# Performance work log

Measured on AMD Instinct MI355X. Metric: run time of the kernel, lower is better.

## Reference

```python
import jax, jax.numpy as jnp
import numpy as np
from jax import lax

VOCAB = 28996  # bert-base-cased vocab size (static for segment_sum)
B, S, D = 32, 512, 768
NUM_CLASSES = 9


def _lstm_dir(x, w_ih, w_hh, b_ih, b_hh):
    # x: [T, N, In]; torch gate order i, f, g, o packed along dim 0 of weights
    T, N, _ = x.shape
    H = w_hh.shape[1]
    xg = jnp.einsum('tni,gi->tng', x, w_ih) + b_ih  # precompute input projections [T,N,4H]

    def step(carry, xg_t):
        h, c = carry
        g = xg_t + h @ w_hh.T + b_hh
        i, f, gg, o = jnp.split(g, 4, axis=-1)
        c = jax.nn.sigmoid(f) * c + jax.nn.sigmoid(i) * jnp.tanh(gg)
        h = jax.nn.sigmoid(o) * jnp.tanh(c)
        return (h, c), h

    h0 = jnp.zeros((N, H), x.dtype)
    _, ys = lax.scan(step, (h0, h0), xg)
    return ys  # [T, N, H]


def setup_inputs() -> dict:
    key = jax.random.key(0)
    ks = jax.random.split(key, 8)
    H, In = D, 2 * D
    w = 0.02
    return {
        'batch': jax.random.randint(ks[0], (B, S), 0, VOCAB),
        'hidden': jax.random.normal(ks[1], (B, S, D), jnp.float32),
        'w_ih_f': jax.random.normal(ks[2], (4 * H, In), jnp.float32) * w,
        'w_hh_f': jax.random.normal(ks[3], (4 * H, H), jnp.float32) * w,
        'b_ih_f': jnp.zeros((4 * H,), jnp.float32),
        'b_hh_f': jnp.zeros((4 * H,), jnp.float32),
        'w_ih_b': jax.random.normal(ks[4], (4 * H, In), jnp.float32) * w,
        'w_hh_b': jax.random.normal(ks[5], (4 * H, H), jnp.float32) * w,
        'b_ih_b': jnp.zeros((4 * H,), jnp.float32),
        'b_hh_b': jnp.zeros((4 * H,), jnp.float32),
        'lin_w': jax.random.normal(ks[6], (NUM_CLASSES, 2 * H), jnp.float32) * w,
        'lin_b': jnp.zeros((NUM_CLASSES,), jnp.float32),
    }


def reference(batch, hidden, w_ih_f, w_hh_f, b_ih_f, b_hh_f,
              w_ih_b, w_hh_b, b_ih_b, b_hh_b, lin_w, lin_b):
    b, s, d = hidden.shape
    flat_ids = batch.reshape(-1)            # [B*S]
    flat_h = hidden.reshape(-1, d)          # [B*S, D]
    # segment mean of embeddings grouped by raw token id (the dict loop in torch)
    sums = jax.ops.segment_sum(flat_h, flat_ids, num_segments=VOCAB)
    counts = jax.ops.segment_sum(jnp.ones((flat_ids.shape[0], 1), hidden.dtype),
                                 flat_ids, num_segments=VOCAB)
    means = sums / jnp.maximum(counts, 1.0)
    ctx = means[flat_ids].reshape(b, s, d)  # gather-broadcast back per position
    x = jnp.concatenate([hidden, ctx], axis=2)  # [B, S, 2D]
    # nn.LSTM is not batch_first: scans over dim0 (B acts as time, S as batch)
    out_f = _lstm_dir(x, w_ih_f, w_hh_f, b_ih_f, b_hh_f)
    out_b = _lstm_dir(x[::-1], w_ih_b, w_hh_b, b_ih_b, b_hh_b)[::-1]
    out = jnp.concatenate([out_f, out_b], axis=-1)  # [B, S, 2D]
    # dropout is identity in eval mode
    return out @ lin_w.T + lin_b  # [B, S, num_classes]
```

## Files before the change

kernel.cpp:

```cpp
#include <hip/hip_runtime.h>

#define VOCAB 28996
#define BB 32
#define SS 512
#define DD 768
#define NCLS 9
#define ROWS (BB*SS)
#define IN2 (2*DD)
#define G4 (4*DD)
#define NB2 (2*G4)

typedef __attribute__((ext_vector_type(8))) short short8;
typedef __attribute__((ext_vector_type(4))) short shortx4;
typedef __attribute__((ext_vector_type(4))) float floatx4;
typedef unsigned long long ull;

__device__ __forceinline__ float bf2f(unsigned short u){
  union { unsigned int i; float f; } v; v.i = ((unsigned int)u) << 16; return v.f;
}
__device__ __forceinline__ unsigned short f2bf(float f){
  union { float f; unsigned int i; } v; v.f = f;
  unsigned int r = v.i + 0x7FFFu + ((v.i >> 16) & 1u);
  return (unsigned short)(r >> 16);
}
__device__ __forceinline__ float sigf(float x){ return 1.0f / (1.0f + __expf(-x)); }
__device__ __forceinline__ float tanhfast(float x){
  float y = fminf(fmaxf(x, -15.f), 15.f);
  float e = __expf(2.f * y);
  return 1.f - 2.f / (e + 1.f);
}

__device__ __forceinline__ void gl_lds16(const unsigned short* g, unsigned short* l){
  __builtin_amdgcn_global_load_lds((__attribute__((address_space(1))) void*)(g),
                                   (__attribute__((address_space(3))) void*)(l), 16, 0, 0);
}
__device__ __forceinline__ void gl_lds16_c(const unsigned short* g, unsigned short* l){
  __builtin_amdgcn_global_load_lds((__attribute__((address_space(1))) void*)(g),
                                   (__attribute__((address_space(3))) void*)(l), 16, 0, 17);
}
__device__ __forceinline__ void store16_sc1(unsigned short* p, short8 v){
  asm volatile("global_store_dwordx4 %0, %1, off sc0 sc1" :: "v"(p), "v"(v) : "memory");
}

#define VMCNT(n) do { asm volatile("s_waitcnt vmcnt(" #n ")" ::: "memory"); \
                      __builtin_amdgcn_sched_barrier(0); } while (0)

__global__ void seg_scatter(const int* __restrict__ ids, const float* __restrict__ hidden,
                            float* __restrict__ sums, float* __restrict__ counts)
{
  int r = blockIdx.x;
  int id = ids[r];
  const float* h = hidden + (long)r * DD;
  float* s = sums + (long)id * DD;
  for (int d = threadIdx.x; d < DD; d += 256)
    atomicAdd(&s[d], h[d]);
  if (threadIdx.x == 0) atomicAdd(&counts[id], 1.0f);
}

__global__ void build_x(const int* __restrict__ ids, const float* __restrict__ hidden,
                        const float* __restrict__ sums, const float* __restrict__ counts,
                        unsigned short* __restrict__ x)
{
  int r = blockIdx.x;
  int id = ids[r];
  float inv = 1.0f / fmaxf(counts[id], 1.0f);
  const float* h = hidden + (long)r * DD;
  const float* s = sums + (long)id * DD;
  unsigned short* xr = x + (long)r * IN2;
  for (int d = threadIdx.x; d < DD; d += 256) {
    xr[d]      = f2bf(h[d]);
    xr[DD + d] = f2bf(s[d] * inv);
  }
}

__global__ void conv_w_perm(const float* __restrict__ w, unsigned short* __restrict__ o, int K)
{
  long i = (long)blockIdx.x * 256 + threadIdx.x;
  if (i >= (long)G4 * K) return;
  int row = (int)(i / K); int k = (int)(i - (long)row * K);
  int u = row >> 2, g = row & 3;
  o[i] = f2bf(w[((long)(g * DD + u)) * K + k]);
}

__global__ void conv_bias_perm(const float* __restrict__ bif, const float* __restrict__ bhf,
                               const float* __restrict__ bib, const float* __restrict__ bhb,
                               float* __restrict__ o)
{
  int n = blockIdx.x * 256 + threadIdx.x;
  if (n >= NB2) return;
  int d = n / G4, rr = n - d * G4, u = rr >> 2, g = rr & 3;
  int s = g * DD + u;
  o[n] = d ? (bib[s] + bhb[s]) : (bif[s] + bhf[s]);
}

__global__ __launch_bounds__(256, 2)
void gemm_bt(const unsigned short* __restrict__ A, int lda,
             const unsigned short* __restrict__ B, int ldb,
             unsigned short* __restrict__ C, int ldc,
             const float* __restrict__ bias, int K)
{
  __shared__ unsigned short lA[128 * 32];
  __shared__ unsigned short lB[128 * 32];
  const int t = threadIdx.x;
  const int lane = t & 63;
  const int wv = t >> 6;
  const int wm = wv >> 1, wn = wv & 1;
  const int l15 = lane & 15, q = lane >> 4;
  const long m0 = (long)blockIdx.y * 128;
  const long n0 = (long)blockIdx.x * 128;
  const int rowS = t >> 2;
  const int kc = (((t & 3) ^ ((t >> 3) & 3))) * 8;
  const int qsw = (q ^ ((l15 >> 1) & 3)) * 8;
  const unsigned short* gA = A + (m0 + rowS) * lda + kc;
  const unsigned short* gB = B + (n0 + rowS) * ldb + kc;
  unsigned short* dA0 = lA + (wv << 9);
  unsigned short* dA1 = lA + 2048 + (wv << 9);
  unsigned short* dB0 = lB + (wv << 9);
  unsigned short* dB1 = lB + 2048 + (wv << 9);

  floatx4 acc[4][4];
  #pragma unroll
  for (int i = 0; i < 4; i++)
    #pragma unroll
    for (int j = 0; j < 4; j++)
      acc[i][j] = (floatx4){0.f, 0.f, 0.f, 0.f};

  const long a64 = (long)64 * lda;
  const long b64 = (long)64 * ldb;
  for (int kt = 0; kt < K; kt += 32) {
    gl_lds16(gA + kt,       dA0);
    gl_lds16(gA + a64 + kt, dA1);
    gl_lds16(gB + kt,       dB0);
    gl_lds16(gB + b64 + kt, dB1);
    __syncthreads();
    short8 af[4], bfr[4];
    #pragma unroll
    for (int i = 0; i < 4; i++)
      af[i] = *(const short8*)(lA + (wm * 64 + i * 16 + l15) * 32 + qsw);
    #pragma unroll
    for (int j = 0; j < 4; j++)
      bfr[j] = *(const short8*)(lB + (wn * 64 + j * 16 + l15) * 32 + qsw);
    #pragma unroll
    for (int i = 0; i < 4; i++)
      #pragma unroll
      for (int j = 0; j < 4; j++)
        acc[i][j] = __builtin_amdgcn_mfma_f32_16x16x32_bf16(af[i], bfr[j], acc[i][j], 0, 0, 0);
    __syncthreads();
  }

  #pragma unroll
  for (int i = 0; i < 4; i++) {
    #pragma unroll
    for (int j = 0; j < 4; j++) {
      const long mg = m0 + wm * 64 + i * 16 + q * 4;
      const long ng = n0 + wn * 64 + j * 16 + l15;
      const float bb = bias[ng];
      #pragma unroll
      for (int r = 0; r < 4; r++)
        C[(mg + r) * ldc + ng] = f2bf(acc[i][j][r] + bb);
    }
  }
}

__global__ __launch_bounds__(512, 1)
void lstm_persist(const unsigned short* __restrict__ xg, int ldxg,
                  const unsigned short* __restrict__ whh,
                  unsigned short* __restrict__ hbuf,
                  unsigned short* __restrict__ outc,
                  unsigned* bar,
                  int dir0, int ndir)
{
  __shared__ unsigned short bufA[16384];
  __shared__ unsigned short bufB[16384];
  __shared__ unsigned short xgs[2][16384];
  __shared__ unsigned short hout[128 * 40];

  const int bid = blockIdx.x;
  const int xcd = bid & 7;
  const int idx = bid >> 3;
  int dm, k3;
  if (ndir == 2) { dm = idx & 7; k3 = idx >> 3; }
  else           { dm = idx & 3; k3 = idx >> 2; }
  const int ld  = (ndir == 2) ? (dm & 1) : 0;
  const int dir = dir0 + ld;
  const int mt  = (ndir == 2) ? (dm >> 1) : dm;
  const int nt  = k3 * 8 + xcd;
  const int m0 = mt * 128, n0 = nt * 128;
  const int u0 = n0 >> 2;
  unsigned* gbar = bar + dm * 16;
  const int nb24 = 24;

  const int t0 = threadIdx.x;
  const int lane = t0 & 63;
  const int wv = t0 >> 6;
  const int wm = wv >> 1;
  const int wn = wv & 1;
  const int l15 = lane & 15, q = lane >> 4;
  const long ldoff = (ndir == 2 && ld == 1) ? (long)G4 : 0;

  const unsigned short* Bdir = whh + (long)dir * G4 * DD;
  const int srow  = lane >> 2;
  const int scolA = (((lane & 3) ^ ((lane >> 3) & 3))) * 8;
  const int qsw   = (q ^ ((l15 >> 1) & 3)) * 8;
  const int xsw   = l15 << 3;
  const int xsrc  = (((t0 & 15) ^ ((t0 >> 4) & 15))) * 8;

  const int rb = wv * 16 + srow;
  const unsigned short* wB  = Bdir + (long)(n0 + rb) * DD + scolA;
  const unsigned short* hA0 = hbuf + ((long)0 * ndir + ld) * ((long)SS * DD) + (long)(m0 + rb) * DD + scolA;
  const unsigned short* hA1 = hbuf + ((long)1 * ndir + ld) * ((long)SS * DD) + (long)(m0 + rb) * DD + scolA;
  unsigned short* dstA = bufA + wv * 512 + lane * 8;
  unsigned short* dstB = bufB + wv * 512 + lane * 8;

  float c_reg[2][4];
  #pragma unroll
  for (int i = 0; i < 2; i++)
    #pragma unroll
    for (int j = 0; j < 4; j++)
      c_reg[i][j] = 0.f;

  {
    const int tt0 = dir ? (BB - 1) : 0;
    const unsigned short* xrow = xg + ((long)tt0 * SS + m0) * ldxg + ldoff + n0;
    #pragma unroll
    for (int c = 0; c < 4; c++) {
      int row = c * 32 + (t0 >> 4);
      gl_lds16(xrow + (long)row * ldxg + xsrc,
               xgs[0] + c * 4096 + (t0 >> 4) * 128 + (t0 & 15) * 8);
    }
  }

  for (int s = 0; s < BB; s++) {
    const int tt = dir ? (BB - 1 - s) : s;
    const unsigned short* hA = (s & 1) ? hA1 : hA0;
    unsigned short* hw = hbuf + (((long)((s + 1) & 1)) * ndir + ld) * ((long)SS * DD);
    const unsigned short* xcur = xgs[s & 1];

    {
      gl_lds16_c(hA,        dstA);
      gl_lds16_c(hA + 32,   dstA + 4096);
      gl_lds16 (wB,         dstB);
      gl_lds16 (wB + 32,    dstB + 4096);
      gl_lds16_c(hA + 64,   dstA + 8192);
      gl_lds16_c(hA + 96,   dstA + 12288);
      gl_lds16 (wB + 64,    dstB + 8192);
      gl_lds16 (wB + 96,    dstB + 12288);
      if (s < BB - 1) {
        const int tn = dir ? (BB - 2 - s) : (s + 1);
        const unsigned short* xrow = xg + ((long)tn * SS + m0) * ldxg + ldoff + n0;
        unsigned short* xnxt = xgs[(s + 1) & 1];
        #pragma unroll
        for (int c = 0; c < 4; c++) {
          int row = c * 32 + (t0 >> 4);
          gl_lds16(xrow + (long)row * ldxg + xsrc,
                   xnxt + c * 4096 + (t0 >> 4) * 128 + (t0 & 15) * 8);
        }
      }
    }
    VMCNT(8);
    __builtin_amdgcn_s_barrier();

    floatx4 acc[2][4];
    #pragma unroll
    for (int i = 0; i < 2; i++)
      #pragma unroll
      for (int j = 0; j < 4; j++)
        acc[i][j] = (floatx4){0.f, 0.f, 0.f, 0.f};

    #pragma unroll
    for (int kt = 0; kt < 12; kt++) {
      const int cur = kt & 1;
      const unsigned short* pA = bufA + cur * 8192;
      const unsigned short* pB = bufB + cur * 8192;
      #pragma unroll
      for (int ks = 0; ks < 2; ks++) {
        short8 af[2], bfr[4];
        #pragma unroll
        for (int i = 0; i < 2; i++)
          af[i] = *(const short8*)(pA + ks * 4096 + (wm * 32 + i * 16 + l15) * 32 + qsw);
        #pragma unroll
        for (int j = 0; j < 4; j++)
          bfr[j] = *(const short8*)(pB + ks * 4096 + (wn * 64 + j * 16 + l15) * 32 + qsw);
        #pragma unroll
        for (int i = 0; i < 2; i++)
          #pragma unroll
          for (int j = 0; j < 4; j++)
            acc[i][j] = __builtin_amdgcn_mfma_f32_16x16x32_bf16(bfr[j], af[i], acc[i][j], 0, 0, 0);
      }
      __builtin_amdgcn_s_barrier();
      if (kt < 10) {
        const long kb = (long)(kt + 2) * 64;
        unsigned short* dA = bufA + cur * 8192 + wv * 512 + lane * 8;
        unsigned short* dB = bufB + cur * 8192 + wv * 512 + lane * 8;
        gl_lds16_c(hA + kb,      dA);
        gl_lds16_c(hA + kb + 32, dA + 4096);
        gl_lds16 (wB + kb,      dB);
        gl_lds16 (wB + kb + 32, dB + 4096);
        VMCNT(4);
        __builtin_amdgcn_s_barrier();
      } else if (kt == 10) {
        VMCNT(0);
        __builtin_amdgcn_s_barrier();
      }
    }

    #pragma unroll
    for (int i = 0; i < 2; i++) {
      const int mrow = wm * 32 + i * 16 + l15;
      const int xbase = mrow * 128;
      #pragma unroll
      for (int j = 0; j < 4; j++) {
        const int nb = wn * 64 + j * 16 + q * 4;
        shortx4 xv = *(const shortx4*)(xcur + xbase + (nb ^ xsw));
        float gi = acc[i][j][0] + bf2f((unsigned short)xv[0]);
        float gf = acc[i][j][1] + bf2f((unsigned short)xv[1]);
        float gg = acc[i][j][2] + bf2f((unsigned short)xv[2]);
        float go = acc[i][j][3] + bf2f((unsigned short)xv[3]);
        float c = sigf(gf) * c_reg[i][j] + sigf(gi) * tanhfast(gg);
        float h = sigf(go) * tanhfast(c);
        c_reg[i][j] = c;
        hout[mrow * 40 + (nb >> 2)] = f2bf(h);
      }
    }
    __syncthreads();
    {
      const int row = t0 >> 2;
      const int qq = t0 & 3;
      short8 v0 = *(const short8*)(hout + row * 40 + qq * 8);
      unsigned short* hwp = hw + (long)(m0 + row) * DD + u0 + qq * 8;
      unsigned short* op  = outc + ((long)tt * SS + m0 + row) * IN2 + dir * DD + u0 + qq * 8;
      store16_sc1(hwp, v0);
      *(short8*)op = v0;
    }
    if (s < BB - 1) {
      VMCNT(0);
      __builtin_amdgcn_s_barrier();
      if (threadIdx.x == 0) {
        unsigned g = __hip_atomic_load(gbar + 1, __ATOMIC_RELAXED, __HIP_MEMORY_SCOPE_AGENT);
        unsigned a = __hip_atomic_fetch_add(gbar, 1u, __ATOMIC_RELAXED, __HIP_MEMORY_SCOPE_AGENT);
        if (a == (unsigned)(nb24 - 1)) {
          __hip_atomic_store(gbar, 0u, __ATOMIC_RELAXED, __HIP_MEMORY_SCOPE_AGENT);
          __hip_atomic_store(gbar + 1, g + 1u, __ATOMIC_RELEASE, __HIP_MEMORY_SCOPE_AGENT);
        } else {
          unsigned curv;
          do {
            __builtin_amdgcn_s_sleep(2);
            curv = __hip_atomic_load(gbar + 1, __ATOMIC_RELAXED, __HIP_MEMORY_SCOPE_AGENT);
          } while (curv == g);
        }
      }
      __builtin_amdgcn_s_barrier();
    }
  }
}

__global__ void final_linear(const unsigned short* __restrict__ xin, const float* __restrict__ w,
                             const float* __restrict__ b, float* __restrict__ out)
{
  __shared__ float red[NCLS * 256];
  int row = blockIdx.x;
  const unsigned short* x = xin + (long)row * IN2;
  float p[NCLS];
  #pragma unroll
  for (int c = 0; c < NCLS; c++) p[c] = 0.f;
  for (int k = threadIdx.x; k < IN2; k += 256) {
    float xv = bf2f(x[k]);
    #pragma unroll
    for (int c = 0; c < NCLS; c++) p[c] += xv * w[c * IN2 + k];
  }
  #pragma unroll
  for (int c = 0; c < NCLS; c++) red[c * 256 + threadIdx.x] = p[c];
  __syncthreads();
  for (int s = 128; s > 0; s >>= 1) {
    if (threadIdx.x < s) {
      #pragma unroll
      for (int c = 0; c < NCLS; c++)
        red[c * 256 + threadIdx.x] += red[c * 256 + threadIdx.x + s];
    }
    __syncthreads();
  }
  if (threadIdx.x < NCLS)
    out[(long)row * NCLS + threadIdx.x] = red[threadIdx.x * 256] + b[threadIdx.x];
}

extern "C" void kernel_launch(void* const* d_in, const int* in_sizes, int n_in,
                              void* d_out, int out_size, void* d_ws, size_t ws_size,
                              hipStream_t stream)
{
  const int*   batch  = (const int*)d_in[0];
  const float* hidden = (const float*)d_in[1];
  const float* w_ih_f = (const float*)d_in[2];
  const float* w_hh_f = (const float*)d_in[3];
  const float* b_ih_f = (const float*)d_in[4];
  const float* b_hh_f = (const float*)d_in[5];
  const float* w_ih_b = (const float*)d_in[6];
  const float* w_hh_b = (const float*)d_in[7];
  const float* b_ih_b = (const float*)d_in[8];
  const float* b_hh_b = (const float*)d_in[9];
  const float* lin_w  = (const float*)d_in[10];
  const float* lin_b  = (const float*)d_in[11];
  float* out = (float*)d_out;

  char* ws = (char*)d_ws;
  size_t off = 0;
  auto alloc = [&](size_t bytes) -> char* {
    char* p = ws + off;
    off += (bytes + 255) & ~(size_t)255;
    return p;
  };

  const size_t SZ_XG_A = (size_t)ROWS * NB2 * 2;
  const size_t SZ_XG_B = (size_t)ROWS * G4  * 2;
  const size_t SZ_XBF  = (size_t)ROWS * IN2 * 2;
  const size_t SZ_W    = (size_t)G4 * IN2 * 2;
  const size_t SZ_BIAS = (size_t)NB2 * 4;
  const size_t SZ_HBUF = (size_t)2 * 2 * SS * DD * 2;
  const size_t SZ_BAR  = 512;
  const size_t SZ_SUMS = (size_t)VOCAB * DD * 4 + (size_t)VOCAB * 4;

  const size_t NEED_C = SZ_XG_A + SZ_XBF + SZ_W + SZ_BIAS + SZ_HBUF + SZ_BAR + 8 * 256;
  const bool combined = ws_size >= NEED_C;

  const long nWIH = (long)G4 * IN2;
  const long nWHH = (long)G4 * DD;

  if (combined) {
    unsigned short* xg   = (unsigned short*)alloc(SZ_XG_A);
    unsigned short* xbf  = (unsigned short*)alloc(SZ_XBF);
    unsigned short* wbuf = (unsigned short*)alloc(SZ_W);
    float*          bias = (float*)alloc(SZ_BIAS);
    unsigned short* hbuf = (unsigned short*)alloc(SZ_HBUF);
    unsigned*       bar  = (unsigned*)alloc(SZ_BAR);
    float* sums   = (float*)xg;
    float* counts = sums + (size_t)VOCAB * DD;

    hipMemsetAsync(sums, 0, SZ_SUMS, stream);
    hipMemsetAsync(bar, 0, SZ_BAR, stream);
    seg_scatter<<<ROWS, 256, 0, stream>>>(batch, hidden, sums, counts);
    build_x<<<ROWS, 256, 0, stream>>>(batch, hidden, sums, counts, xbf);
    conv_bias_perm<<<(NB2 + 255) / 256, 256, 0, stream>>>(b_ih_f, b_hh_f, b_ih_b, b_hh_b, bias);

    for (int dir = 0; dir < 2; dir++) {
      conv_w_perm<<<(unsigned)((nWIH + 255) / 256), 256, 0, stream>>>(dir ? w_ih_b : w_ih_f, wbuf, IN2);
      dim3 grid(G4 / 128, ROWS / 128, 1);
      gemm_bt<<<grid, 256, 0, stream>>>(xbf, IN2, wbuf, IN2,
                                        xg + (size_t)dir * G4, NB2,
                                        bias + (size_t)dir * G4, IN2);
    }
    conv_w_perm<<<(unsigned)((nWHH + 255) / 256), 256, 0, stream>>>(w_hh_f, wbuf, DD);
    conv_w_perm<<<(unsigned)((nWHH + 255) / 256), 256, 0, stream>>>(w_hh_b, wbuf + (size_t)G4 * DD, DD);

    hipMemsetAsync(hbuf, 0, SZ_HBUF, stream);
    lstm_persist<<<192, 512, 0, stream>>>(xg, NB2, wbuf, hbuf, xbf, bar, 0, 2);
    final_linear<<<ROWS, 256, 0, stream>>>(xbf, lin_w, lin_b, out);
  } else {
    unsigned short* xg   = (unsigned short*)alloc(SZ_XG_B);
    unsigned short* xbf  = (unsigned short*)alloc(SZ_XBF);
    unsigned short* outc = (unsigned short*)alloc(SZ_XBF);
    unsigned short* wih  = (unsigned short*)alloc(SZ_W);
    unsigned short* whh  = (unsigned short*)alloc(SZ_W);
    float*          bias = (float*)alloc(SZ_BIAS);
    unsigned short* hbuf = (unsigned short*)alloc(SZ_HBUF);
    unsigned*       bar  = (unsigned*)alloc(SZ_BAR);
    float* sums   = (float*)xg;
    float* counts = sums + (size_t)VOCAB * DD;

    hipMemsetAsync(sums, 0, SZ_SUMS, stream);
    hipMemsetAsync(bar, 0, SZ_BAR, stream);
    seg_scatter<<<ROWS, 256, 0, stream>>>(batch, hidden, sums, counts);
    build_x<<<ROWS, 256, 0, stream>>>(batch, hidden, sums, counts, xbf);
    conv_bias_perm<<<(NB2 + 255) / 256, 256, 0, stream>>>(b_ih_f, b_hh_f, b_ih_b, b_hh_b, bias);
    conv_w_perm<<<(unsigned)((nWHH + 255) / 256), 256, 0, stream>>>(w_hh_f, whh, DD);
    conv_w_perm<<<(unsigned)((nWHH + 255) / 256), 256, 0, stream>>>(w_hh_b, whh + (size_t)G4 * DD, DD);

    for (int dir = 0; dir < 2; dir++) {
      conv_w_perm<<<(unsigned)((nWIH + 255) / 256), 256, 0, stream>>>(dir ? w_ih_b : w_ih_f, wih, IN2);
      {
        dim3 grid(G4 / 128, ROWS / 128, 1);
        gemm_bt<<<grid, 256, 0, stream>>>(xbf, IN2, wih, IN2, xg, G4,
                                          bias + (size_t)dir * G4, IN2);
      }
      hipMemsetAsync(hbuf, 0, SZ_HBUF, stream);
      lstm_persist<<<96, 512, 0, stream>>>(xg, G4, whh, hbuf, outc, bar, dir, 1);
    }
    final_linear<<<ROWS, 256, 0, stream>>>(outc, lin_w, lin_b, out);
  }
}
```

Measured before the change: 1.225 ms.

## Restructure LSTM recurrent K-loop into 6 double-buffered chunks with register xg loads

The persistent LSTM kernel's per-step recurrent GEMM now uses two full K=128 LDS buffers for h and W_hh instead of split 64-wide halves, giving 6 outer iterations with one prefetch and fewer barriers per iteration. The precomputed input-gate values are loaded straight into registers from global memory rather than staged through a double-buffered LDS array, which frees LDS for the larger h/W buffers. It also raises wave priority around the MFMA section. The direct global loads of xg may be less coalesced and add register pressure, and their latency now sits in the step's critical path instead of being prefetched a step ahead.

```diff
diff --git a/kernel.cpp b/kernel.cpp
--- a/kernel.cpp
+++ b/kernel.cpp
@@ -170,9 +170,8 @@
                   unsigned* bar,
                   int dir0, int ndir)
 {
-  __shared__ unsigned short bufA[16384];
-  __shared__ unsigned short bufB[16384];
-  __shared__ unsigned short xgs[2][16384];
+  __shared__ unsigned short bufA[2][16384];
+  __shared__ unsigned short bufB[2][16384];
   __shared__ unsigned short hout[128 * 40];
 
   const int bid = blockIdx.x;
@@ -202,15 +201,11 @@
   const int srow  = lane >> 2;
   const int scolA = (((lane & 3) ^ ((lane >> 3) & 3))) * 8;
   const int qsw   = (q ^ ((l15 >> 1) & 3)) * 8;
-  const int xsw   = l15 << 3;
-  const int xsrc  = (((t0 & 15) ^ ((t0 >> 4) & 15))) * 8;
 
   const int rb = wv * 16 + srow;
   const unsigned short* wB  = Bdir + (long)(n0 + rb) * DD + scolA;
   const unsigned short* hA0 = hbuf + ((long)0 * ndir + ld) * ((long)SS * DD) + (long)(m0 + rb) * DD + scolA;
   const unsigned short* hA1 = hbuf + ((long)1 * ndir + ld) * ((long)SS * DD) + (long)(m0 + rb) * DD + scolA;
-  unsigned short* dstA = bufA + wv * 512 + lane * 8;
-  unsigned short* dstB = bufB + wv * 512 + lane * 8;
 
   float c_reg[2][4];
   #pragma unroll
@@ -218,47 +213,28 @@
     #pragma unroll
     for (int j = 0; j < 4; j++)
       c_reg[i][j] = 0.f;
-
-  {
-    const int tt0 = dir ? (BB - 1) : 0;
-    const unsigned short* xrow = xg + ((long)tt0 * SS + m0) * ldxg + ldoff + n0;
-    #pragma unroll
-    for (int c = 0; c < 4; c++) {
-      int row = c * 32 + (t0 >> 4);
-      gl_lds16(xrow + (long)row * ldxg + xsrc,
-               xgs[0] + c * 4096 + (t0 >> 4) * 128 + (t0 & 15) * 8);
-    }
-  }
 
   for (int s = 0; s < BB; s++) {
     const int tt = dir ? (BB - 1 - s) : s;
     const unsigned short* hA = (s & 1) ? hA1 : hA0;
     unsigned short* hw = hbuf + (((long)((s + 1) & 1)) * ndir + ld) * ((long)SS * DD);
-    const unsigned short* xcur = xgs[s & 1];
-
+
+    #pragma unroll
+    for (int p = 0; p < 4; p++) {
+      gl_lds16_c(hA + p * 32, &bufA[0][p * 4096 + wv * 512 + lane * 8]);
+      gl_lds16 (wB + p * 32, &bufB[0][p * 4096 + wv * 512 + lane * 8]);
+    }
+    shortx4 xr0[4], xr1[4];
     {
-      gl_lds16_c(hA,        dstA);
-      gl_lds16_c(hA + 32,   dstA + 4096);
-      gl_lds16 (wB,         dstB);
-      gl_lds16 (wB + 32,    dstB + 4096);
-      gl_lds16_c(hA + 64,   dstA + 8192);
-      gl_lds16_c(hA + 96,   dstA + 12288);
-      gl_lds16 (wB + 64,    dstB + 8192);
-      gl_lds16 (wB + 96,    dstB + 12288);
-      if (s < BB - 1) {
-        const int tn = dir ? (BB - 2 - s) : (s + 1);
-        const unsigned short* xrow = xg + ((long)tn * SS + m0) * ldxg + ldoff + n0;
-        unsigned short* xnxt = xgs[(s + 1) & 1];
-        #pragma unroll
-        for (int c = 0; c < 4; c++) {
-          int row = c * 32 + (t0 >> 4);
-          gl_lds16(xrow + (long)row * ldxg + xsrc,
-                   xnxt + c * 4096 + (t0 >> 4) * 128 + (t0 & 15) * 8);
-        }
-      }
-    }
-    VMCNT(8);
-    __builtin_amdgcn_s_barrier();
+      const unsigned short* xb = xg + ((long)tt * SS + m0) * ldxg + ldoff + n0;
+      const unsigned short* xb0 = xb + (long)(wm * 32 + l15) * ldxg + wn * 64 + q * 4;
+      const unsigned short* xb1 = xb0 + (long)16 * ldxg;
+      #pragma unroll
+      for (int j = 0; j < 4; j++) {
+        xr0[j] = *(const shortx4*)(xb0 + j * 16);
+        xr1[j] = *(const shortx4*)(xb1 + j * 16);
+      }
+    }
 
     floatx4 acc[2][4];
     #pragma unroll
@@ -268,50 +244,50 @@
         acc[i][j] = (floatx4){0.f, 0.f, 0.f, 0.f};
 
     #pragma unroll
-    for (int kt = 0; kt < 12; kt++) {
-      const int cur = kt & 1;
-      const unsigned short* pA = bufA + cur * 8192;
-      const unsigned short* pB = bufB + cur * 8192;
-      #pragma unroll
-      for (int ks = 0; ks < 2; ks++) {
+    for (int j6 = 0; j6 < 6; j6++) {
+      if (j6 < 5) {
+        const int b = (j6 + 1) & 1;
+        const long kb = (long)(j6 + 1) * 128;
+        #pragma unroll
+        for (int p = 0; p < 4; p++) {
+          gl_lds16_c(hA + kb + p * 32, &bufA[b][p * 4096 + wv * 512 + lane * 8]);
+          gl_lds16 (wB + kb + p * 32, &bufB[b][p * 4096 + wv * 512 + lane * 8]);
+        }
+      }
+      if (j6 == 0)      VMCNT(16);
+      else if (j6 < 5)  VMCNT(8);
+      else              VMCNT(0);
+      __builtin_amdgcn_s_barrier();
+      const int b = j6 & 1;
+      __builtin_amdgcn_s_setprio(1);
+      #pragma unroll
+      for (int ks = 0; ks < 4; ks++) {
+        const unsigned short* pA = &bufA[b][ks * 4096];
+        const unsigned short* pB = &bufB[b][ks * 4096];
         short8 af[2], bfr[4];
         #pragma unroll
         for (int i = 0; i < 2; i++)
-          af[i] = *(const short8*)(pA + ks * 4096 + (wm * 32 + i * 16 + l15) * 32 + qsw);
+          af[i] = *(const short8*)(pA + (wm * 32 + i * 16 + l15) * 32 + qsw);
         #pragma unroll
         for (int j = 0; j < 4; j++)
-          bfr[j] = *(const short8*)(pB + ks * 4096 + (wn * 64 + j * 16 + l15) * 32 + qsw);
+          bfr[j] = *(const short8*)(pB + (wn * 64 + j * 16 + l15) * 32 + qsw);
         #pragma unroll
         for (int i = 0; i < 2; i++)
           #pragma unroll
           for (int j = 0; j < 4; j++)
             acc[i][j] = __builtin_amdgcn_mfma_f32_16x16x32_bf16(bfr[j], af[i], acc[i][j], 0, 0, 0);
       }
-      __builtin_amdgcn_s_barrier();
-      if (kt < 10) {
-        const long kb = (long)(kt + 2) * 64;
-        unsigned short* dA = bufA + cur * 8192 + wv * 512 + lane * 8;
-        unsigned short* dB = bufB + cur * 8192 + wv * 512 + lane * 8;
-        gl_lds16_c(hA + kb,      dA);
-        gl_lds16_c(hA + kb + 32, dA + 4096);
-        gl_lds16 (wB + kb,      dB);
-        gl_lds16 (wB + kb + 32, dB + 4096);
-        VMCNT(4);
-        __builtin_amdgcn_s_barrier();
-      } else if (kt == 10) {
-        VMCNT(0);
-        __builtin_amdgcn_s_barrier();
-      }
+      __builtin_amdgcn_s_setprio(0);
+      if (j6 < 5) __builtin_amdgcn_s_barrier();
     }
 
     #pragma unroll
     for (int i = 0; i < 2; i++) {
       const int mrow = wm * 32 + i * 16 + l15;
-      const int xbase = mrow * 128;
       #pragma unroll
       for (int j = 0; j < 4; j++) {
         const int nb = wn * 64 + j * 16 + q * 4;
-        shortx4 xv = *(const shortx4*)(xcur + xbase + (nb ^ xsw));
+        shortx4 xv = i ? xr1[j] : xr0[j];
         float gi = acc[i][j][0] + bf2f((unsigned short)xv[0]);
         float gf = acc[i][j][1] + bf2f((unsigned short)xv[1]);
         float gg = acc[i][j][2] + bf2f((unsigned short)xv[2]);
```

Measured after the change: 1.235 ms. Within noise of the previous version (+0.8%).
